# Optimization experiments

Hardware: AMD Instinct MI355X
Metric: run time of the kernel (lower is better)

Reference implementation:

```python
import jax, jax.numpy as jnp
import numpy as np

# model_grid_shape (flipped ensemble grid, all equal here); E = 8 experts
GRID = (2, 2, 2)
E = GRID[0] * GRID[1] * GRID[2]
N = 524288   # query points
H = 64       # sub-model MLP hidden width


def setup_inputs() -> dict:
    key = jax.random.key(0)
    ks = jax.random.split(key, 4)
    # query coordinates in [-1, 1]^3
    x = jax.random.uniform(ks[0], (N, 3), jnp.float32, -1.0, 1.0)
    # per-expert spatial extents: axis-aligned cells tiling [-1,1]^3, in the
    # same flat order as the routing index i0 + i1*g0 + i2*g0*g1
    i = np.arange(E)
    cell = np.stack([i % GRID[0], (i // GRID[0]) % GRID[1],
                     i // (GRID[0] * GRID[1])], axis=-1).astype(np.float32)
    g = np.array(GRID, np.float32)
    extents_min = jnp.asarray(-1.0 + 2.0 * cell / g)          # [E, 3]
    extents_max = jnp.asarray(-1.0 + 2.0 * (cell + 1.0) / g)  # [E, 3]
    # per-expert SRN MLP parameters: 3 -> H -> H -> 1
    W1 = jax.random.normal(ks[1], (E, 3, H), jnp.float32) / np.sqrt(3.0)
    b1 = jnp.zeros((E, H), jnp.float32)
    W2 = jax.random.normal(ks[2], (E, H, H), jnp.float32) / np.sqrt(float(H))
    b2 = jnp.zeros((E, H), jnp.float32)
    W3 = jax.random.normal(ks[3], (E, H, 1), jnp.float32) / np.sqrt(float(H))
    b3 = jnp.zeros((E, 1), jnp.float32)
    return {"x": x, "extents_min": extents_min, "extents_max": extents_max,
            "W1": W1, "b1": b1, "W2": W2, "b2": b2, "W3": W3, "b3": b3}


def reference(x, extents_min, extents_max, W1, b1, W2, b2, W3, b3):
    # --- routing: flat expert index per point (matches torch forward) ---
    u = jnp.clip((x + 1.0) * 0.5, 0.0, 0.99)
    gvec = jnp.asarray(GRID, x.dtype)
    gi = (u * gvec).astype(jnp.int32)                       # [N, 3]
    idx = gi[:, 0] + gi[:, 1] * GRID[0] + gi[:, 2] * (GRID[0] * GRID[1])

    # --- dispatch/combine: scan over experts, masked scatter into y ---
    def body(y, args):
        i, emin, emax, w1, bb1, w2, bb2, w3, bb3 = args
        # normalize point into expert-local [-1, 1]^3
        xn = -1.0 + 2.0 * ((x - emin) / (emax - emin))      # [N, 3]
        h = jax.nn.relu(xn @ w1 + bb1)                      # [N, H]
        h = jax.nn.relu(h @ w2 + bb2)                       # [N, H]
        o = h @ w3 + bb3                                    # [N, 1]
        mask = (idx == i)[:, None]
        return jnp.where(mask, o, y), None

    y0 = jnp.zeros((x.shape[0], 1), x.dtype)
    y, _ = jax.lax.scan(
        body, y0,
        (jnp.arange(E), extents_min, extents_max, W1, b1, W2, b2, W3, b3))
    return y
```

## Files before the change

kernel.cpp:

```cpp
#include <hip/hip_runtime.h>

typedef __bf16 bf16x8 __attribute__((ext_vector_type(8)));
typedef __bf16 bf16x2 __attribute__((ext_vector_type(2)));
typedef float f32x4 __attribute__((ext_vector_type(4)));
typedef float f32x2 __attribute__((ext_vector_type(2)));

#define N_PTS 524288
#define SBLK 256
#define PTS_PER_SBLK 2048
#define CAP 73728
#define POISON 0xAAAAAAAAu

__device__ __forceinline__ unsigned short f2bf(float f) {
    unsigned u = __float_as_uint(f);
    u += 0x7FFFu + ((u >> 16) & 1u);
    return (unsigned short)(u >> 16);
}

__device__ __forceinline__ unsigned decode(unsigned c) {
    return (c >= POISON) ? (c - POISON) : c;
}

__device__ __forceinline__ int route(float x0, float x1, float x2) {
    int g0 = (int)(fminf(fmaxf((x0 + 1.0f) * 0.5f, 0.0f), 0.99f) * 2.0f);
    int g1 = (int)(fminf(fmaxf((x1 + 1.0f) * 0.5f, 0.0f), 0.99f) * 2.0f);
    int g2 = (int)(fminf(fmaxf((x2 + 1.0f) * 0.5f, 0.0f), 0.99f) * 2.0f);
    return g0 + 2*g1 + 4*g2;
}

#define OFF_CNT  0u
#define OFF_W1P  1024u
#define OFF_EP   10240u
#define OFF_W2F  16384u
#define OFF_XG   131072u

extern "C" __global__ void __launch_bounds__(256) k3_scatter(
        const float* __restrict__ x, int* __restrict__ cursor,
        float4* __restrict__ xg,
        const float* __restrict__ emin, const float* __restrict__ emax,
        const float* __restrict__ W1, const float* __restrict__ b1,
        const float* __restrict__ W2, const float* __restrict__ b2,
        const float* __restrict__ W3,
        float4* __restrict__ W1P, float2* __restrict__ EP,
        uint4* __restrict__ W2F) {
    int t = threadIdx.x;

    if (blockIdx.x >= SBLK) {
        int e = blockIdx.x - SBLK;
        if (t < 64) {
            int n = t;
            float d0 = emax[e*3+0] - emin[e*3+0];
            float d1 = emax[e*3+1] - emin[e*3+1];
            float d2 = emax[e*3+2] - emin[e*3+2];
            float a0 = 2.0f/d0, a1 = 2.0f/d1, a2 = 2.0f/d2;
            float cc0 = -1.0f - 2.0f*emin[e*3+0]/d0;
            float cc1 = -1.0f - 2.0f*emin[e*3+1]/d1;
            float cc2 = -1.0f - 2.0f*emin[e*3+2]/d2;
            float w0 = W1[(e*3+0)*64 + n];
            float w1 = W1[(e*3+1)*64 + n];
            float w2 = W1[(e*3+2)*64 + n];
            float4 w;
            w.x = a0*w0; w.y = a1*w1; w.z = a2*w2;
            w.w = cc0*w0 + cc1*w1 + cc2*w2 + b1[e*64 + n];
            W1P[e*64 + n] = w;
            EP[e*64 + n] = make_float2(b2[e*64 + n], W3[e*64 + n]);
        }
        #pragma unroll
        for (int s = 0; s < 2; ++s) {
            int q  = s*256 + t;
            int fi = q >> 6, l = q & 63;
            int mt = fi >> 1, kt = fi & 1;
            int n  = mt*16 + (l & 15);
            int g8 = (l >> 4) * 8;
            union { unsigned short us[8]; uint4 u4; } v;
            #pragma unroll
            for (int j = 0; j < 8; ++j)
                v.us[j] = f2bf(W2[(e*64 + kt*32 + g8 + j)*64 + n]);
            W2F[(e*8 + fi)*64 + l] = v.u4;
        }
        return;
    }

    __shared__ int lh[8];
    __shared__ int startS[8];
    if (t < 8) lh[t] = 0;
    __syncthreads();
    int base = blockIdx.x * PTS_PER_SBLK;
    float c0[8], c1[8], c2[8];
    int rnk[8];
    unsigned epack = 0;
    #pragma unroll
    for (int i = 0; i < 8; ++i) {
        int p = base + i * 256 + t;
        c0[i] = x[3*p]; c1[i] = x[3*p+1]; c2[i] = x[3*p+2];
        int e = route(c0[i], c1[i], c2[i]);
        epack |= (unsigned)e << (3*i);
        rnk[i] = atomicAdd(&lh[e], 1);
    }
    __syncthreads();
    if (t < 8) {
        unsigned claim = (unsigned)atomicAdd(&cursor[t], lh[t]);
        startS[t] = (int)decode(claim);
    }
    __syncthreads();
    #pragma unroll
    for (int i = 0; i < 8; ++i) {
        int e = (epack >> (3*i)) & 7;
        float4 v;
        v.x = c0[i]; v.y = c1[i]; v.z = c2[i];
        v.w = __uint_as_float((unsigned)(base + i * 256 + t));
        xg[e*CAP + startS[e] + rnk[i]] = v;
    }
}

extern "C" __global__ void __launch_bounds__(256, 3) k4_mlp(
        const float4* __restrict__ xg, const int* __restrict__ cursor,
        const float4* __restrict__ W1P, const float2* __restrict__ EP,
        const bf16x8* __restrict__ W2F, const float* __restrict__ b3,
        float* __restrict__ y) {
    int e = blockIdx.y;
    int cnt = (int)decode((unsigned)cursor[e]);
    int tileStart = blockIdx.x * 256;
    if (tileStart >= cnt) return;

    int t = threadIdx.x;
    int lane = t & 63, wave = t >> 6;
    int m16 = lane & 15;
    int g  = lane >> 4;
    int g8 = g * 8;

    __shared__ __align__(16) unsigned short h1s[256][72];

    bf16x8 A[4][2];
    #pragma unroll
    for (int mt = 0; mt < 4; ++mt)
        #pragma unroll
        for (int kt = 0; kt < 2; ++kt)
            A[mt][kt] = W2F[(e*8 + mt*2 + kt)*64 + lane];

    int valid = (tileStart + t) < cnt;
    float px = 0.f, py = 0.f, pz = 0.f;
    unsigned pidx = 0;
    if (valid) {
        float4 v = xg[e*CAP + tileStart + t];
        px = v.x; py = v.y; pz = v.z; pidx = __float_as_uint(v.w);
    }

    #pragma unroll
    for (int jb = 0; jb < 8; ++jb) {
        bf16x8 hv;
        #pragma unroll
        for (int j2 = 0; j2 < 8; j2 += 2) {
            float4 wa = W1P[e*64 + jb*8 + j2];
            float4 wb = W1P[e*64 + jb*8 + j2 + 1];
            float ha = fmaf(px, wa.x, fmaf(py, wa.y, fmaf(pz, wa.z, wa.w)));
            float hb = fmaf(px, wb.x, fmaf(py, wb.y, fmaf(pz, wb.z, wb.w)));
            f32x2 hp;
            hp[0] = fmaxf(ha, 0.0f);
            hp[1] = fmaxf(hb, 0.0f);
            bf16x2 bp = __builtin_convertvector(hp, bf16x2);
            hv[j2] = bp[0]; hv[j2+1] = bp[1];
        }
        *(bf16x8*)(&h1s[t][jb*8]) = hv;
    }

    asm volatile("s_waitcnt lgkmcnt(0)" ::: "memory");

    f32x4 acc[4][4] = {};
    #pragma unroll
    for (int pt = 0; pt < 4; ++pt) {
        int row = wave*64 + pt*16 + m16;
        bf16x8 B0 = *(const bf16x8*)(&h1s[row][g8]);
        bf16x8 B1 = *(const bf16x8*)(&h1s[row][32 + g8]);
        #pragma unroll
        for (int mt = 0; mt < 4; ++mt) {
            acc[mt][pt] = __builtin_amdgcn_mfma_f32_16x16x32_bf16(A[mt][0], B0, acc[mt][pt], 0, 0, 0);
            acc[mt][pt] = __builtin_amdgcn_mfma_f32_16x16x32_bf16(A[mt][1], B1, acc[mt][pt], 0, 0, 0);
        }
    }

    float s0 = 0.f, s1 = 0.f, s2 = 0.f, s3 = 0.f;
    #pragma unroll
    for (int mt = 0; mt < 4; ++mt) {
        #pragma unroll
        for (int r = 0; r < 4; ++r) {
            float2 ep = EP[e*64 + mt*16 + g*4 + r];
            s0 = fmaf(fmaxf(acc[mt][0][r] + ep.x, 0.f), ep.y, s0);
            s1 = fmaf(fmaxf(acc[mt][1][r] + ep.x, 0.f), ep.y, s1);
            s2 = fmaf(fmaxf(acc[mt][2][r] + ep.x, 0.f), ep.y, s2);
            s3 = fmaf(fmaxf(acc[mt][3][r] + ep.x, 0.f), ep.y, s3);
        }
    }
    float bb3 = b3[e];
    float sv[4] = {s0, s1, s2, s3};
    #pragma unroll
    for (int pt = 0; pt < 4; ++pt) {
        float s = sv[pt];
        s += __shfl_xor(s, 16, 64);
        s += __shfl_xor(s, 32, 64);
        unsigned oi = (unsigned)__shfl((int)pidx, pt*16 + m16, 64);
        int row = wave*64 + pt*16 + m16;
        if (lane < 16 && (tileStart + row) < cnt) {
            y[oi] = s + bb3;
        }
    }
}

extern "C" void kernel_launch(void* const* d_in, const int* in_sizes, int n_in,
                              void* d_out, int out_size, void* d_ws, size_t ws_size,
                              hipStream_t stream) {
    const float* x    = (const float*)d_in[0];
    const float* emin = (const float*)d_in[1];
    const float* emax = (const float*)d_in[2];
    const float* W1   = (const float*)d_in[3];
    const float* b1   = (const float*)d_in[4];
    const float* W2   = (const float*)d_in[5];
    const float* b2   = (const float*)d_in[6];
    const float* W3   = (const float*)d_in[7];
    const float* b3   = (const float*)d_in[8];
    float* y = (float*)d_out;

    char* ws = (char*)d_ws;
    int*    cursor = (int*)(ws + OFF_CNT);
    float4* W1P    = (float4*)(ws + OFF_W1P);
    float2* EP     = (float2*)(ws + OFF_EP);
    uint4*  W2F    = (uint4*)(ws + OFF_W2F);
    float4* xg     = (float4*)(ws + OFF_XG);

    k3_scatter<<<SBLK + 8, 256, 0, stream>>>(x, cursor, xg, emin, emax,
                                             W1, b1, W2, b2, W3, W1P, EP, W2F);
    k4_mlp<<<dim3(288, 8), 256, 0, stream>>>(xg, cursor, W1P, EP,
                                             (const bf16x8*)W2F, b3, y);
}
```

Before: 94.66 us.

## Compute layer-1 activations directly in MFMA B-fragment registers and vectorize scatter loads

The MLP kernel no longer stages layer-1 activations through shared memory. Each lane loads the points it needs for its B fragments and computes the 16-channel slices of h1 in registers, which duplicates the layer-1 math four times across lane groups. The scatter kernel now launches twice as many blocks with four points per thread, read as three contiguous float4 loads, and the point index encoding changes to match. The gain is no LDS traffic or barrier, paid for with redundant FMAs and more scalar/vector W1P loads per lane.

```diff
diff --git a/kernel.cpp b/kernel.cpp
--- a/kernel.cpp
+++ b/kernel.cpp
@@ -6,8 +6,8 @@
 typedef float f32x2 __attribute__((ext_vector_type(2)));
 
 #define N_PTS 524288
-#define SBLK 256
-#define PTS_PER_SBLK 2048
+#define SBLK 512
+#define PTS_PER_SBLK 1024
 #define CAP 73728
 #define POISON 0xAAAAAAAAu
 
@@ -86,13 +86,18 @@
     if (t < 8) lh[t] = 0;
     __syncthreads();
     int base = blockIdx.x * PTS_PER_SBLK;
-    float c0[8], c1[8], c2[8];
-    int rnk[8];
+
+    const float4* x4 = (const float4*)x;
+    int fb = blockIdx.x * 768 + t * 3;
+    float4 q0 = x4[fb], q1 = x4[fb+1], q2 = x4[fb+2];
+    float c0[4] = {q0.x, q0.w, q1.z, q2.y};
+    float c1[4] = {q0.y, q1.x, q1.w, q2.z};
+    float c2[4] = {q0.z, q1.y, q2.x, q2.w};
+
+    int rnk[4];
     unsigned epack = 0;
     #pragma unroll
-    for (int i = 0; i < 8; ++i) {
-        int p = base + i * 256 + t;
-        c0[i] = x[3*p]; c1[i] = x[3*p+1]; c2[i] = x[3*p+2];
+    for (int i = 0; i < 4; ++i) {
         int e = route(c0[i], c1[i], c2[i]);
         epack |= (unsigned)e << (3*i);
         rnk[i] = atomicAdd(&lh[e], 1);
@@ -104,11 +109,11 @@
     }
     __syncthreads();
     #pragma unroll
-    for (int i = 0; i < 8; ++i) {
+    for (int i = 0; i < 4; ++i) {
         int e = (epack >> (3*i)) & 7;
         float4 v;
         v.x = c0[i]; v.y = c1[i]; v.z = c2[i];
-        v.w = __uint_as_float((unsigned)(base + i * 256 + t));
+        v.w = __uint_as_float((unsigned)(base + 4*t + i));
         xg[e*CAP + startS[e] + rnk[i]] = v;
     }
 }
@@ -129,8 +134,6 @@
     int g  = lane >> 4;
     int g8 = g * 8;
 
-    __shared__ __align__(16) unsigned short h1s[256][72];
-
     bf16x8 A[4][2];
     #pragma unroll
     for (int mt = 0; mt < 4; ++mt)
@@ -138,44 +141,35 @@
         for (int kt = 0; kt < 2; ++kt)
             A[mt][kt] = W2F[(e*8 + mt*2 + kt)*64 + lane];
 
-    int valid = (tileStart + t) < cnt;
-    float px = 0.f, py = 0.f, pz = 0.f;
-    unsigned pidx = 0;
-    if (valid) {
-        float4 v = xg[e*CAP + tileStart + t];
-        px = v.x; py = v.y; pz = v.z; pidx = __float_as_uint(v.w);
-    }
-
-    #pragma unroll
-    for (int jb = 0; jb < 8; ++jb) {
-        bf16x8 hv;
-        #pragma unroll
-        for (int j2 = 0; j2 < 8; j2 += 2) {
-            float4 wa = W1P[e*64 + jb*8 + j2];
-            float4 wb = W1P[e*64 + jb*8 + j2 + 1];
-            float ha = fmaf(px, wa.x, fmaf(py, wa.y, fmaf(pz, wa.z, wa.w)));
-            float hb = fmaf(px, wb.x, fmaf(py, wb.y, fmaf(pz, wb.z, wb.w)));
-            f32x2 hp;
-            hp[0] = fmaxf(ha, 0.0f);
-            hp[1] = fmaxf(hb, 0.0f);
-            bf16x2 bp = __builtin_convertvector(hp, bf16x2);
-            hv[j2] = bp[0]; hv[j2+1] = bp[1];
-        }
-        *(bf16x8*)(&h1s[t][jb*8]) = hv;
-    }
-
-    asm volatile("s_waitcnt lgkmcnt(0)" ::: "memory");
-
+    int rowBase = tileStart + wave*64 + m16;
+    float4 c[4];
+    #pragma unroll
+    for (int pt = 0; pt < 4; ++pt)
+        c[pt] = xg[e*CAP + rowBase + pt*16];
+
+    const float4* __restrict__ wb = W1P + e*64;
     f32x4 acc[4][4] = {};
-    #pragma unroll
-    for (int pt = 0; pt < 4; ++pt) {
-        int row = wave*64 + pt*16 + m16;
-        bf16x8 B0 = *(const bf16x8*)(&h1s[row][g8]);
-        bf16x8 B1 = *(const bf16x8*)(&h1s[row][32 + g8]);
-        #pragma unroll
-        for (int mt = 0; mt < 4; ++mt) {
-            acc[mt][pt] = __builtin_amdgcn_mfma_f32_16x16x32_bf16(A[mt][0], B0, acc[mt][pt], 0, 0, 0);
-            acc[mt][pt] = __builtin_amdgcn_mfma_f32_16x16x32_bf16(A[mt][1], B1, acc[mt][pt], 0, 0, 0);
+
+    #pragma unroll
+    for (int half = 0; half < 2; ++half) {
+        #pragma unroll
+        for (int pt = 0; pt < 4; ++pt) {
+            bf16x8 B;
+            #pragma unroll
+            for (int j = 0; j < 8; j += 2) {
+                float4 wa = wb[half*32 + g8 + j];
+                float4 wv = wb[half*32 + g8 + j + 1];
+                float ha = fmaf(c[pt].x, wa.x, fmaf(c[pt].y, wa.y, fmaf(c[pt].z, wa.z, wa.w)));
+                float hb = fmaf(c[pt].x, wv.x, fmaf(c[pt].y, wv.y, fmaf(c[pt].z, wv.z, wv.w)));
+                f32x2 hp;
+                hp[0] = fmaxf(ha, 0.0f);
+                hp[1] = fmaxf(hb, 0.0f);
+                bf16x2 bp = __builtin_convertvector(hp, bf16x2);
+                B[j] = bp[0]; B[j+1] = bp[1];
+            }
+            #pragma unroll
+            for (int mt = 0; mt < 4; ++mt)
+                acc[mt][pt] = __builtin_amdgcn_mfma_f32_16x16x32_bf16(A[mt][half], B, acc[mt][pt], 0, 0, 0);
         }
     }
 
@@ -198,10 +192,8 @@
         float s = sv[pt];
         s += __shfl_xor(s, 16, 64);
         s += __shfl_xor(s, 32, 64);
-        unsigned oi = (unsigned)__shfl((int)pidx, pt*16 + m16, 64);
-        int row = wave*64 + pt*16 + m16;
-        if (lane < 16 && (tileStart + row) < cnt) {
-            y[oi] = s + bb3;
+        if (lane < 16 && (rowBase + pt*16) < cnt) {
+            y[__float_as_uint(c[pt].w)] = s + bb3;
         }
     }
 }
```

After: 93.95 us. No clear change (-0.7%).
